# Optimization experiments

Measured on AMD Instinct MI355X. Metric: run time of the kernel, lower is better.

## Reference

```python
import jax, jax.numpy as jnp
import numpy as np

EPS_LN = 1e-5

def layer_norm(x, w, b):
    u = x.mean(-1, keepdims=True)
    s = jnp.mean((x - u) ** 2, -1, keepdims=True)
    return w * ((x - u) / jnp.sqrt(s + EPS_LN)) + b

def mlp(x, W, b, lw, lb):
    return jax.nn.relu(layer_norm(x @ W + b, lw, lb))

def mlp_gate(x, W, b, lw, lb):
    return jax.nn.sigmoid(layer_norm(x @ W + b, lw, lb))

def setup_inputs() -> dict:
    N, D = 768, 64
    key = jax.random.key(0)
    ks = jax.random.split(key, 12)
    inp = {
        'corr_index': jax.random.normal(ks[0], (N, N, 2), jnp.float32),
        'nei_index': jax.random.randint(ks[1], (N, N), 0, 2).astype(jnp.int64),
        'nei_num': jax.random.randint(ks[2], (N,), 0, N).astype(jnp.int64),
        'hidden_state': jax.random.normal(ks[3], (N, D), jnp.float32),
        'agent_v': jax.random.normal(ks[4], (N, 2), jnp.float32),
        # relativeLayer: MLP(3, D)
        'rel_w': jax.random.normal(ks[5], (3, D), jnp.float32) * (1.0 / np.sqrt(3)),
        'rel_b': jnp.zeros((D,), jnp.float32),
        'rel_lw': jnp.ones((D,), jnp.float32),
        'rel_lb': jnp.zeros((D,), jnp.float32),
        # ngate: MLP_gate(3D, D)
        'ng_w': jax.random.normal(ks[6], (3 * D, D), jnp.float32) * (1.0 / np.sqrt(3 * D)),
        'ng_b': jnp.zeros((D,), jnp.float32),
        'ng_lw': jnp.ones((D,), jnp.float32),
        'ng_lb': jnp.zeros((D,), jnp.float32),
        # WAr: MLP(3D, 1) -- LayerNorm(1) is identity in the source
        'war_w': jax.random.normal(ks[7], (3 * D, 1), jnp.float32) * (1.0 / np.sqrt(3 * D)),
        'war_b': jnp.zeros((1,), jnp.float32),
        # weight: MLP(D, D)
        'wt_w': jax.random.normal(ks[8], (D, D), jnp.float32) * (1.0 / np.sqrt(D)),
        'wt_b': jnp.zeros((D,), jnp.float32),
        'wt_lw': jnp.ones((D,), jnp.float32),
        'wt_lb': jnp.zeros((D,), jnp.float32),
    }
    return inp

def reference(corr_index, nei_index, nei_num, hidden_state, agent_v,
              rel_w, rel_b, rel_lw, rel_lb,
              ng_w, ng_b, ng_lw, ng_lb,
              war_w, war_b,
              wt_w, wt_b, wt_lw, wt_lb):
    N, D = hidden_state.shape
    # pair layout: row i*N+j  (i = receiver row of the NxN grid, j = column)
    agent_vt = jnp.tile(agent_v, (N, 1))                     # [N*N, 2], row i*N+j -> agent_v[j]
    corr_t = corr_index.reshape(N * N, 2)
    dot = agent_vt[:, 0] * corr_t[:, 0] + agent_vt[:, 1] * corr_t[:, 1]
    judge = jnp.sum(agent_vt ** 2, -1)
    angle = dot / (jnp.sqrt(judge * jnp.sum(corr_t ** 2, -1)) + 1e-10)
    angle = jnp.where(judge == 0, -1.0, angle)
    corr3 = jnp.concatenate([corr_t, angle[:, None]], -1)    # [N*N, 3]

    r_t = mlp(corr3, rel_w, rel_b, rel_lw, rel_lb)           # [N*N, D]
    nei_inputs = jnp.tile(hidden_state, (N, 1))              # row i*N+j -> h[j]
    hi_t = jnp.repeat(hidden_state, N, axis=0)               # row i*N+j -> h[i]
    tmp = jnp.concatenate([r_t, hi_t, nei_inputs], 1)        # [N*N, 3D]

    mask = (nei_index.reshape(N * N) > 0)
    nGate = mlp_gate(tmp, ng_w, ng_b, ng_lw, ng_lb)          # [N*N, D]
    tt = jax.nn.relu(tmp @ war_w + war_b).reshape(-1)        # LayerNorm(1) == identity

    Pos = jnp.where(mask, tt, 0.0).reshape(N, N)
    Pos = jnp.where(Pos == 0, -10000.0, Pos)
    Pos = jax.nn.softmax(Pos, axis=1)
    Pos_t = Pos.reshape(-1)

    H = jnp.where(mask[:, None], nei_inputs * nGate * Pos_t[:, None], 0.0)
    H_sum = mlp(H.reshape(N, N, D).sum(1), wt_w, wt_b, wt_lw, wt_lb)
    return hidden_state + H_sum
```

## Files before the change

kernel.cpp:

```cpp
#include <hip/hip_runtime.h>
#include <math.h>

#define NN 768
#define DD 64
#define WPB 4
#define HALVES 3
#define JW (NN / HALVES)
#define NSUB 4
#define RSTRIDE 34
#define B1STR 12
#define PREBLKS 18
#define PSTRIDE 68

typedef _Float16 half8 __attribute__((ext_vector_type(8)));
typedef float    f32x4 __attribute__((ext_vector_type(4)));
typedef __fp16   p2f   __attribute__((ext_vector_type(2)));

union FragU { uint4 u4; unsigned int u[4]; half8 h; };
union PkU   { unsigned int u; p2f p; };

__device__ __forceinline__ unsigned int pk2(float a, float b) {
    PkU t; t.p = __builtin_amdgcn_cvt_pkrtz(a, b); return t.u;
}
__device__ __forceinline__ float lane_bcast(float v, int src) {
    return __int_as_float(__builtin_amdgcn_readlane(__float_as_int(v), src));
}
__device__ __forceinline__ float rfl(float v) {
    return __int_as_float(__builtin_amdgcn_readfirstlane(__float_as_int(v)));
}
__device__ __forceinline__ f32x4 mfma16(FragU a, FragU b, f32x4 c) {
    return __builtin_amdgcn_mfma_f32_16x16x32_f16(a.h, b.h, c, 0, 0, 0);
}

__global__ __launch_bounds__(256) void k_prepack(
    const float* __restrict__ hs, const float* __restrict__ ng_w,
    const float* __restrict__ ng_b, const float* __restrict__ war_w,
    const float* __restrict__ war_b,
    const float* __restrict__ rel_w, const float* __restrict__ rel_b,
    const float* __restrict__ rel_lw, const float* __restrict__ rel_lb,
    float* __restrict__ sbase, float* __restrict__ warb, float* __restrict__ war3,
    unsigned int* __restrict__ hf16,
    unsigned int* __restrict__ afragS, unsigned int* __restrict__ afragR,
    float* __restrict__ mom)
{
    const int t = threadIdx.x, blk = blockIdx.x;
    const int lane = t & 63, q = t >> 6, g = lane >> 4, c16 = lane & 15;

    if (blk >= PREBLKS) {
        const int row = (blk - PREBLKS) * 4 + q;
        const float hv = hs[row * DD + lane];
        float a2 = ng_b[lane];
        #pragma unroll 8
        for (int k = 0; k < DD; ++k)
            a2 = fmaf(lane_bcast(hv, k), ng_w[(DD + k) * DD + lane], a2);
        sbase[row * DD + lane] = a2;
        float t2 = hv * war_w[DD + lane];
        float t3 = hv * war_w[2 * DD + lane];
        #pragma unroll
        for (int o = 32; o; o >>= 1) { t2 += __shfl_xor(t2, o); t3 += __shfl_xor(t3, o); }
        if (lane == 0) { warb[row] = t2 + war_b[0]; war3[row] = t3; }
        return;
    }

    for (int idx = blk * 256 + t; idx < NN * 32; idx += PREBLKS * 256) {
        const int row = idx >> 5, c = idx & 31;
        hf16[idx] = pk2(hs[row * DD + 2 * c], hs[row * DD + 2 * c + 1]);
    }

    if (blk < 16) {
        const int b = blk >> 2, c = blk & 3;
        const int dout = 16 * b + c16;
        const int k0 = 32 * c + g * 8 + 2 * q;
        const int r0 = (k0 < 64) ? k0 : (k0 + 64);
        afragS[(blk * 64 + lane) * 4 + q] =
            pk2(ng_w[r0 * DD + dout], ng_w[(r0 + 1) * DD + dout]);
    } else if (blk == 16) {
        const int b = q;
        const int d = 16 * b + c16;
        const float rlwd = rel_lw[d], rlbd = rel_lb[d];
        const float c0 = rel_w[d] * rlwd;
        const float c1 = rel_w[DD + d] * rlwd;
        const float c2 = rel_w[2 * DD + d] * rlwd;
        const float c3 = rel_b[d] * rlwd;
        PkU h01, h23, h45;
        h01.p = __builtin_amdgcn_cvt_pkrtz(c0, c1);
        h23.p = __builtin_amdgcn_cvt_pkrtz(c2, c3);
        h45.p = __builtin_amdgcn_cvt_pkrtz(rlwd, rlbd);
        const unsigned l01 = pk2(c0 - (float)h01.p[0], c1 - (float)h01.p[1]);
        const unsigned l23 = pk2(c2 - (float)h23.p[0], c3 - (float)h23.p[1]);
        const unsigned l45 = pk2(rlwd - (float)h45.p[0], rlbd - (float)h45.p[1]);
        const unsigned int base = (b * 64 + lane) * 4;
        unsigned v0, v1, v2;
        if (g == 0 || g == 1)      { v0 = h01.u; v1 = h23.u; v2 = h45.u; }
        else if (g == 2)           { v0 = l01;   v1 = l23;   v2 = l45;   }
        else                       { v0 = 0u;    v1 = 0u;    v2 = 0u;    }
        afragR[base + 0] = v0;
        afragR[base + 1] = v1;
        afragR[base + 2] = v2;
        afragR[base + 3] = 0u;
    } else {
        if (t < 64) {
            const float x0 = rel_w[t], x1 = rel_w[DD + t], x2 = rel_w[2 * DD + t];
            const float x3 = rel_b[t];
            float v[14] = {x0, x1, x2, x3,
                           x0 * x0, x1 * x1, x2 * x2, x3 * x3,
                           x0 * x1, x0 * x2, x0 * x3, x1 * x2, x1 * x3, x2 * x3};
            #pragma unroll
            for (int qq = 0; qq < 14; ++qq) {
                float s = v[qq];
                #pragma unroll
                for (int o = 32; o; o >>= 1) s += __shfl_xor(s, o);
                if (t == 0) mom[qq] = s * (1.f / 64.f);
            }
        }
    }
}

__global__ __launch_bounds__(64 * WPB) void k_main(
    const float* __restrict__ corr, const int* __restrict__ nei,
    const float* __restrict__ hs, const float* __restrict__ av,
    const float* __restrict__ ng_lw, const float* __restrict__ ng_lb,
    const float* __restrict__ war_w,
    const float* __restrict__ sbase, const float* __restrict__ warb,
    const float* __restrict__ war3,
    const unsigned int* __restrict__ afragS, const unsigned int* __restrict__ afragR,
    const unsigned int* __restrict__ hf16, const float* __restrict__ mom,
    float* __restrict__ part)
{
    const int h = blockIdx.x;
    const int i = blockIdx.y;
    const int tid = threadIdx.x;
    const int lane = tid & 63, wave = tid >> 6;
    const int g = lane >> 4, c16 = lane & 15;

    __shared__ uint4 sm_aS[16 * 64];
    __shared__ __align__(16) float sm_cst[4 * DD];
    __shared__ unsigned int sm_b1[WPB * 64 * B1STR];
    __shared__ unsigned int smr[WPB * 16 * RSTRIDE];
    __shared__ float sm_red[WPB][DD];
    __shared__ float sm_m[WPB], sm_l[WPB];

    for (int f = tid; f < 16 * 64; f += 64 * WPB)
        sm_aS[f] = ((const uint4*)afragS)[f];
    {
        const int a = tid >> 6, d = tid & 63;
        float v;
        if (a == 0)      v = sbase[i * DD + d];
        else if (a == 1) v = war_w[d];
        else if (a == 2) v = ng_lw[d];
        else             v = ng_lb[d];
        sm_cst[a * DD + d] = v;
    }

    FragU aR[4];
    #pragma unroll
    for (int b = 0; b < 4; ++b) aR[b].u4 = ((const uint4*)afragR)[b * 64 + lane];

    const float m0 = rfl(mom[0]), m1 = rfl(mom[1]), m2 = rfl(mom[2]), m3 = rfl(mom[3]);
    const float M00 = rfl(mom[4]), M11 = rfl(mom[5]), M22 = rfl(mom[6]), M33 = rfl(mom[7]);
    const float M01 = rfl(mom[8]), M02 = rfl(mom[9]), M03 = rfl(mom[10]);
    const float M12 = rfl(mom[11]), M13 = rfl(mom[12]), M23 = rfl(mom[13]);
    const float warbase = rfl(warb[i]);

    unsigned int* wrbase = smr + (wave * 16 + c16) * RSTRIDE;

    __syncthreads();

    const int jwbase = h * JW + wave * 64;
    {
        const int j = jwbase + lane;
        const float2 cc = ((const float2*)corr)[i * NN + j];
        const float2 vv = ((const float2*)av)[j];
        const float cx = cc.x, cy = cc.y;
        const float judge = vv.x * vv.x + vv.y * vv.y;
        const float dotv = fmaf(vv.x, cx, vv.y * cy);
        const float cn = cx * cx + cy * cy;
        float angle = __fdividef(dotv, sqrtf(judge * cn) + 1e-10f);
        if (judge == 0.f) angle = -1.f;

        const float u = fmaf(cx, m0, fmaf(cy, m1, fmaf(angle, m2, m3)));
        float e2 = M33;
        e2 = fmaf(cx * cx, M00, e2);
        e2 = fmaf(cy * cy, M11, e2);
        e2 = fmaf(angle * angle, M22, e2);
        e2 = fmaf(2.f * cx, fmaf(cy, M01, fmaf(angle, M02, M03)), e2);
        e2 = fmaf(2.f * cy, fmaf(angle, M12, M13), e2);
        e2 = fmaf(2.f * angle, M23, e2);
        const float vare = (e2 - u * u) + 1e-5f;
        const float inv = rsqrtf(vare);

        const float xc0 = cx * inv, xc1 = cy * inv, xc2 = angle * inv;
        const float xc3 = inv, xc4 = -u * inv;
        PkU s01, s23, s45;
        s01.p = __builtin_amdgcn_cvt_pkrtz(xc0, xc1);
        s23.p = __builtin_amdgcn_cvt_pkrtz(xc2, xc3);
        s45.p = __builtin_amdgcn_cvt_pkrtz(xc4, 1.f);
        const unsigned l0 = pk2(xc0 - (float)s01.p[0], xc1 - (float)s01.p[1]);
        const unsigned l1 = pk2(xc2 - (float)s23.p[0], xc3 - (float)s23.p[1]);
        const unsigned l2 = pk2(xc4 - (float)s45.p[0], 0.f);

        unsigned int* bp = sm_b1 + (wave * 64 + lane) * B1STR;
        *(uint4*)(bp)     = make_uint4(s01.u, s23.u, s45.u, 0u);
        *(uint4*)(bp + 4) = make_uint4(l0, l1, l2, 0u);
    }

    float acc[16];
    #pragma unroll
    for (int x = 0; x < 16; ++x) acc[x] = 0.f;
    float mrun = -INFINITY, lrun = 0.f;

    unsigned zofs = 0;

    #pragma unroll 1
    for (int s = 0; s < NSUB; ++s) {
        asm volatile("" : "+v"(zofs));
        const uint4* aSp = sm_aS + zofs;
        const float* cst = sm_cst + zofs;

        const int jj = jwbase + 16 * s + c16;
        const int    nv = nei[i * NN + jj];
        const float  w3 = war3[jj];
        FragU bx2, bx3;
        bx2.u4 = *(const uint4*)(hf16 + jj * 32 + 4 * g);
        bx3.u4 = *(const uint4*)(hf16 + jj * 32 + 16 + 4 * g);

        FragU b1;
        {
            const unsigned int* bp =
                sm_b1 + (wave * 64 + 16 * s + c16) * B1STR + ((g == 1) ? 4 : 0);
            const uint4 w = *(const uint4*)bp;
            b1.u[0] = (g == 3) ? 0u : w.x;
            b1.u[1] = (g == 3) ? 0u : w.y;
            b1.u[2] = (g == 3) ? 0u : w.z;
            b1.u[3] = 0u;
        }

        const f32x4 Z = {0.f, 0.f, 0.f, 0.f};
        float wd = 0.f;
        #pragma unroll
        for (int b = 0; b < 4; ++b) {
            const f32x4 P = mfma16(aR[b], b1, Z);
            const f32x4 wv = *(const f32x4*)(cst + 1 * DD + 16 * b + 4 * g);
            const float r0f = fmaxf(P[0], 0.f);
            const float r1f = fmaxf(P[1], 0.f);
            const float r2f = fmaxf(P[2], 0.f);
            const float r3f = fmaxf(P[3], 0.f);
            wd = fmaf(r0f, wv[0], wd);
            wd = fmaf(r1f, wv[1], wd);
            wd = fmaf(r2f, wv[2], wd);
            wd = fmaf(r3f, wv[3], wd);
            uint2 wvv;
            wvv.x = pk2(r0f, r1f);
            wvv.y = pk2(r2f, r3f);
            *(uint2*)(wrbase + 8 * b + 2 * g) = wvv;
        }

        FragU bx0, bx1;
        {
            const uint2 lo0 = *(const uint2*)(wrbase + 4 * g);
            const uint2 hi0 = *(const uint2*)(wrbase + 4 * g + 2);
            bx0.u[0] = lo0.x; bx0.u[1] = lo0.y; bx0.u[2] = hi0.x; bx0.u[3] = hi0.y;
            const uint2 lo1 = *(const uint2*)(wrbase + 16 + 4 * g);
            const uint2 hi1 = *(const uint2*)(wrbase + 16 + 4 * g + 2);
            bx1.u[0] = lo1.x; bx1.u[1] = lo1.y; bx1.u[2] = hi1.x; bx1.u[3] = hi1.y;
        }

        const f32x4 hv0 = *(const f32x4*)(hs + jj * DD +  0 + 4 * g);
        const f32x4 hv1 = *(const f32x4*)(hs + jj * DD + 16 + 4 * g);
        const f32x4 hv2 = *(const f32x4*)(hs + jj * DD + 32 + 4 * g);
        const f32x4 hv3 = *(const f32x4*)(hs + jj * DD + 48 + 4 * g);

        wd += __shfl_xor(wd, 16);
        wd += __shfl_xor(wd, 32);

        f32x4 S[4];
        #pragma unroll
        for (int b = 0; b < 4; ++b) {
            f32x4 cinit = *(const f32x4*)(cst + 0 * DD + 16 * b + 4 * g);
            FragU a2f, a3f, a0f, a1f;
            a2f.u4 = aSp[(b * 4 + 2) * 64 + lane];
            a3f.u4 = aSp[(b * 4 + 3) * 64 + lane];
            a0f.u4 = aSp[(b * 4 + 0) * 64 + lane];
            a1f.u4 = aSp[(b * 4 + 1) * 64 + lane];
            cinit = mfma16(a2f, bx2, cinit);
            cinit = mfma16(a3f, bx3, cinit);
            cinit = mfma16(a0f, bx0, cinit);
            cinit = mfma16(a1f, bx1, cinit);
            S[b] = cinit;
        }

        float s1 = 0.f, s2 = 0.f;
        #pragma unroll
        for (int x = 0; x < 16; ++x) {
            const float sv = S[x >> 2][x & 3];
            s1 += sv; s2 = fmaf(sv, sv, s2);
        }
        s1 += __shfl_xor(s1, 16); s1 += __shfl_xor(s1, 32);
        s2 += __shfl_xor(s2, 16); s2 += __shfl_xor(s2, 32);
        const float u2 = s1 * (1.f / 64.f);
        const float var2 = fmaf(s2, 1.f / 64.f, -u2 * u2);
        const float inv2 = rsqrtf(var2 + 1e-5f);

        float tt = wd + w3 + warbase;
        tt = fmaxf(tt, 0.f);
        const bool msk = nv > 0;
        const float p = (msk && tt > 0.f) ? tt : -10000.f;

        const float mn = fmaxf(mrun, p);
        const float alpha = __expf(mrun - mn);
        const float e = __expf(p - mn);
        const float eacc = msk ? e : 0.f;
        lrun = fmaf(lrun, alpha, e);
        mrun = mn;

        #pragma unroll
        for (int b = 0; b < 4; ++b) {
            const f32x4 hvb = (b == 0) ? hv0 : (b == 1) ? hv1 : (b == 2) ? hv2 : hv3;
            const f32x4 lw = *(const f32x4*)(cst + 2 * DD + 16 * b + 4 * g);
            const f32x4 lb = *(const f32x4*)(cst + 3 * DD + 16 * b + 4 * g);
            #pragma unroll
            for (int r = 0; r < 4; ++r) {
                const float ngv = fmaf((S[b][r] - u2) * inv2, lw[r], lb[r]);
                const float gate = __fdividef(1.f, 1.f + __expf(-ngv));
                acc[b * 4 + r] = fmaf(acc[b * 4 + r], alpha, eacc * gate * hvb[r]);
            }
        }
    }

    #pragma unroll
    for (int o = 1; o <= 8; o <<= 1) {
        const float mo  = __shfl_xor(mrun, o);
        const float lo_ = __shfl_xor(lrun, o);
        const float M   = fmaxf(mrun, mo);
        const float a1  = __expf(mrun - M);
        const float a2  = __expf(mo - M);
        lrun = lrun * a1 + lo_ * a2;
        #pragma unroll
        for (int x = 0; x < 16; ++x) {
            const float ao = __shfl_xor(acc[x], o);
            acc[x] = acc[x] * a1 + ao * a2;
        }
        mrun = M;
    }
    if (c16 == 0) {
        #pragma unroll
        for (int b = 0; b < 4; ++b)
            #pragma unroll
            for (int r = 0; r < 4; ++r)
                sm_red[wave][16 * b + g * 4 + r] = acc[b * 4 + r];
        if (lane == 0) { sm_m[wave] = mrun; sm_l[wave] = lrun; }
    }
    __syncthreads();

    if (tid < DD) {
        float M = sm_m[0];
        #pragma unroll
        for (int w = 1; w < WPB; ++w) M = fmaxf(M, sm_m[w]);
        float L = 0.f, A = 0.f;
        #pragma unroll
        for (int w = 0; w < WPB; ++w) {
            const float f = __expf(sm_m[w] - M);
            L = fmaf(sm_l[w], f, L);
            A = fmaf(sm_red[w][tid], f, A);
        }
        float* p = part + (i * HALVES + h) * PSTRIDE;
        p[tid] = A;
        if (tid == 0) { p[64] = M; p[65] = L; }
    }
}

__global__ __launch_bounds__(64) void k_final(
    const float* __restrict__ hs, const float* __restrict__ part,
    const float* __restrict__ wt_w, const float* __restrict__ wt_b,
    const float* __restrict__ wt_lw, const float* __restrict__ wt_lb,
    float* __restrict__ out)
{
    const int i = blockIdx.x;
    const int tid = threadIdx.x;

    float ms[HALVES], ls[HALVES];
    float M = -INFINITY;
    #pragma unroll
    for (int hh = 0; hh < HALVES; ++hh) {
        const float* p = part + (i * HALVES + hh) * PSTRIDE;
        ms[hh] = p[64]; ls[hh] = p[65];
        M = fmaxf(M, ms[hh]);
    }
    float L = 0.f, A = 0.f;
    #pragma unroll
    for (int hh = 0; hh < HALVES; ++hh) {
        const float f = __expf(ms[hh] - M);
        L = fmaf(ls[hh], f, L);
        A = fmaf(part[(i * HALVES + hh) * PSTRIDE + tid], f, A);
    }
    const float Hv = A / L;

    float v = wt_b[tid];
    #pragma unroll 8
    for (int k = 0; k < DD; ++k)
        v = fmaf(lane_bcast(Hv, k), wt_w[k * DD + tid], v);
    float t1 = v, t2 = v * v;
    #pragma unroll
    for (int o = 32; o; o >>= 1) { t1 += __shfl_xor(t1, o); t2 += __shfl_xor(t2, o); }
    const float uo = t1 * (1.f / 64.f);
    const float varo = fmaf(t2, 1.f / 64.f, -uo * uo);
    const float invo = rsqrtf(varo + 1e-5f);
    const float ro = fmaf((v - uo) * invo, wt_lw[tid], wt_lb[tid]);
    out[i * DD + tid] = hs[i * DD + tid] + fmaxf(ro, 0.f);
}

extern "C" void kernel_launch(void* const* d_in, const int* in_sizes, int n_in,
                              void* d_out, int out_size, void* d_ws, size_t ws_size,
                              hipStream_t stream) {
    const float* corr   = (const float*)d_in[0];
    const int*   nei    = (const int*)  d_in[1];
    const float* hs     = (const float*)d_in[3];
    const float* av     = (const float*)d_in[4];
    const float* rel_w  = (const float*)d_in[5];
    const float* rel_b  = (const float*)d_in[6];
    const float* rel_lw = (const float*)d_in[7];
    const float* rel_lb = (const float*)d_in[8];
    const float* ng_w   = (const float*)d_in[9];
    const float* ng_b   = (const float*)d_in[10];
    const float* ng_lw  = (const float*)d_in[11];
    const float* ng_lb  = (const float*)d_in[12];
    const float* war_w  = (const float*)d_in[13];
    const float* war_b  = (const float*)d_in[14];
    const float* wt_w   = (const float*)d_in[15];
    const float* wt_b   = (const float*)d_in[16];
    const float* wt_lw  = (const float*)d_in[17];
    const float* wt_lb  = (const float*)d_in[18];
    float* out = (float*)d_out;

    float* ws    = (float*)d_ws;
    float* sbase = ws;
    float* warb  = sbase + NN * DD;
    float* war3  = warb + NN;
    float* mom   = war3 + NN;
    unsigned int* hf16   = (unsigned int*)(mom + 16);
    unsigned int* afragS = hf16 + NN * 32;
    unsigned int* afragR = afragS + 16 * 64 * 4;
    float* part  = (float*)(afragR + 4 * 64 * 4);

    k_prepack<<<PREBLKS + NN / 4, 256, 0, stream>>>(
        hs, ng_w, ng_b, war_w, war_b, rel_w, rel_b, rel_lw, rel_lb,
        sbase, warb, war3, hf16, afragS, afragR, mom);
    k_main<<<dim3(HALVES, NN), 64 * WPB, 0, stream>>>(
        corr, nei, hs, av, ng_lw, ng_lb, war_w, sbase, warb, war3,
        afragS, afragR, hf16, mom, part);
    k_final<<<NN, 64, 0, stream>>>(
        hs, part, wt_w, wt_b, wt_lw, wt_lb, out);
}
```

Baseline: 144.9 us.

## Fuse final MLP into main kernel via last-block atomic counter

Removes the separate k_final launch. Each k_main block increments a per-row counter, and the last block for that row merges the softmax partials and runs the output MLP and LayerNorm. The counters are zeroed in the prepack kernel. It also splits the padded b1 shared buffer into two uint4 arrays and refactors the LayerNorm and gate arithmetic into fewer ops. The cost is a threadfence and atomic per block, plus a serial tail on the last block of each row.

```diff
diff --git a/kernel.cpp b/kernel.cpp
--- a/kernel.cpp
+++ b/kernel.cpp
@@ -8,7 +8,6 @@
 #define JW (NN / HALVES)
 #define NSUB 4
 #define RSTRIDE 34
-#define B1STR 12
 #define PREBLKS 18
 #define PSTRIDE 68
 
@@ -41,7 +40,7 @@
     float* __restrict__ sbase, float* __restrict__ warb, float* __restrict__ war3,
     unsigned int* __restrict__ hf16,
     unsigned int* __restrict__ afragS, unsigned int* __restrict__ afragR,
-    float* __restrict__ mom)
+    float* __restrict__ mom, unsigned int* __restrict__ cnt)
 {
     const int t = threadIdx.x, blk = blockIdx.x;
     const int lane = t & 63, q = t >> 6, g = lane >> 4, c16 = lane & 15;
@@ -99,6 +98,7 @@
         afragR[base + 2] = v2;
         afragR[base + 3] = 0u;
     } else {
+        for (int idx = t; idx < NN; idx += 256) cnt[idx] = 0u;
         if (t < 64) {
             const float x0 = rel_w[t], x1 = rel_w[DD + t], x2 = rel_w[2 * DD + t];
             const float x3 = rel_b[t];
@@ -125,7 +125,10 @@
     const float* __restrict__ war3,
     const unsigned int* __restrict__ afragS, const unsigned int* __restrict__ afragR,
     const unsigned int* __restrict__ hf16, const float* __restrict__ mom,
-    float* __restrict__ part)
+    float* __restrict__ part, unsigned int* __restrict__ cnt,
+    const float* __restrict__ wt_w, const float* __restrict__ wt_b,
+    const float* __restrict__ wt_lw, const float* __restrict__ wt_lb,
+    float* __restrict__ out)
 {
     const int h = blockIdx.x;
     const int i = blockIdx.y;
@@ -135,10 +138,12 @@
 
     __shared__ uint4 sm_aS[16 * 64];
     __shared__ __align__(16) float sm_cst[4 * DD];
-    __shared__ unsigned int sm_b1[WPB * 64 * B1STR];
+    __shared__ uint4 sm_b1h[WPB * 64];
+    __shared__ uint4 sm_b1l[WPB * 64];
     __shared__ unsigned int smr[WPB * 16 * RSTRIDE];
     __shared__ float sm_red[WPB][DD];
     __shared__ float sm_m[WPB], sm_l[WPB];
+    __shared__ unsigned int sm_last;
 
     for (int f = tid; f < 16 * 64; f += 64 * WPB)
         sm_aS[f] = ((const uint4*)afragS)[f];
@@ -199,9 +204,8 @@
         const unsigned l1 = pk2(xc2 - (float)s23.p[0], xc3 - (float)s23.p[1]);
         const unsigned l2 = pk2(xc4 - (float)s45.p[0], 0.f);
 
-        unsigned int* bp = sm_b1 + (wave * 64 + lane) * B1STR;
-        *(uint4*)(bp)     = make_uint4(s01.u, s23.u, s45.u, 0u);
-        *(uint4*)(bp + 4) = make_uint4(l0, l1, l2, 0u);
+        sm_b1h[wave * 64 + lane] = make_uint4(s01.u, s23.u, s45.u, 0u);
+        sm_b1l[wave * 64 + lane] = make_uint4(l0, l1, l2, 0u);
     }
 
     float acc[16];
@@ -226,9 +230,8 @@
 
         FragU b1;
         {
-            const unsigned int* bp =
-                sm_b1 + (wave * 64 + 16 * s + c16) * B1STR + ((g == 1) ? 4 : 0);
-            const uint4 w = *(const uint4*)bp;
+            const int bi = wave * 64 + 16 * s + c16;
+            const uint4 w = (g == 1) ? sm_b1l[bi] : sm_b1h[bi];
             b1.u[0] = (g == 3) ? 0u : w.x;
             b1.u[1] = (g == 3) ? 0u : w.y;
             b1.u[2] = (g == 3) ? 0u : w.z;
@@ -320,9 +323,12 @@
             const f32x4 lb = *(const f32x4*)(cst + 3 * DD + 16 * b + 4 * g);
             #pragma unroll
             for (int r = 0; r < 4; ++r) {
-                const float ngv = fmaf((S[b][r] - u2) * inv2, lw[r], lb[r]);
+                const float ilw = inv2 * lw[r];
+                const float blb = fmaf(-u2, ilw, lb[r]);
+                const float ngv = fmaf(S[b][r], ilw, blb);
                 const float gate = __fdividef(1.f, 1.f + __expf(-ngv));
-                acc[b * 4 + r] = fmaf(acc[b * 4 + r], alpha, eacc * gate * hvb[r]);
+                const float ehv = eacc * hvb[r];
+                acc[b * 4 + r] = fmaf(acc[b * 4 + r], alpha, gate * ehv);
             }
         }
     }
@@ -367,46 +373,46 @@
         p[tid] = A;
         if (tid == 0) { p[64] = M; p[65] = L; }
     }
-}
-
-__global__ __launch_bounds__(64) void k_final(
-    const float* __restrict__ hs, const float* __restrict__ part,
-    const float* __restrict__ wt_w, const float* __restrict__ wt_b,
-    const float* __restrict__ wt_lw, const float* __restrict__ wt_lb,
-    float* __restrict__ out)
-{
-    const int i = blockIdx.x;
-    const int tid = threadIdx.x;
-
-    float ms[HALVES], ls[HALVES];
-    float M = -INFINITY;
-    #pragma unroll
-    for (int hh = 0; hh < HALVES; ++hh) {
-        const float* p = part + (i * HALVES + hh) * PSTRIDE;
-        ms[hh] = p[64]; ls[hh] = p[65];
-        M = fmaxf(M, ms[hh]);
-    }
-    float L = 0.f, A = 0.f;
-    #pragma unroll
-    for (int hh = 0; hh < HALVES; ++hh) {
-        const float f = __expf(ms[hh] - M);
-        L = fmaf(ls[hh], f, L);
-        A = fmaf(part[(i * HALVES + hh) * PSTRIDE + tid], f, A);
-    }
-    const float Hv = A / L;
-
-    float v = wt_b[tid];
-    #pragma unroll 8
-    for (int k = 0; k < DD; ++k)
-        v = fmaf(lane_bcast(Hv, k), wt_w[k * DD + tid], v);
-    float t1 = v, t2 = v * v;
-    #pragma unroll
-    for (int o = 32; o; o >>= 1) { t1 += __shfl_xor(t1, o); t2 += __shfl_xor(t2, o); }
-    const float uo = t1 * (1.f / 64.f);
-    const float varo = fmaf(t2, 1.f / 64.f, -uo * uo);
-    const float invo = rsqrtf(varo + 1e-5f);
-    const float ro = fmaf((v - uo) * invo, wt_lw[tid], wt_lb[tid]);
-    out[i * DD + tid] = hs[i * DD + tid] + fmaxf(ro, 0.f);
+
+    __threadfence();
+    __syncthreads();
+    if (tid == 0)
+        sm_last = (atomicAdd(&cnt[i], 1u) == HALVES - 1) ? 1u : 0u;
+    __syncthreads();
+    if (sm_last) {
+        __threadfence();
+        if (tid < DD) {
+            float ms[HALVES], ls[HALVES];
+            float M = -INFINITY;
+            #pragma unroll
+            for (int hh = 0; hh < HALVES; ++hh) {
+                const float* p = part + (i * HALVES + hh) * PSTRIDE;
+                ms[hh] = p[64]; ls[hh] = p[65];
+                M = fmaxf(M, ms[hh]);
+            }
+            float L = 0.f, A = 0.f;
+            #pragma unroll
+            for (int hh = 0; hh < HALVES; ++hh) {
+                const float f = __expf(ms[hh] - M);
+                L = fmaf(ls[hh], f, L);
+                A = fmaf(part[(i * HALVES + hh) * PSTRIDE + tid], f, A);
+            }
+            const float Hv = A / L;
+
+            float v = wt_b[tid];
+            #pragma unroll 8
+            for (int k = 0; k < DD; ++k)
+                v = fmaf(lane_bcast(Hv, k), wt_w[k * DD + tid], v);
+            float t1 = v, t2 = v * v;
+            #pragma unroll
+            for (int o = 32; o; o >>= 1) { t1 += __shfl_xor(t1, o); t2 += __shfl_xor(t2, o); }
+            const float uo = t1 * (1.f / 64.f);
+            const float varo = fmaf(t2, 1.f / 64.f, -uo * uo);
+            const float invo = rsqrtf(varo + 1e-5f);
+            const float ro = fmaf((v - uo) * invo, wt_lw[tid], wt_lb[tid]);
+            out[i * DD + tid] = hs[i * DD + tid] + fmaxf(ro, 0.f);
+        }
+    }
 }
 
 extern "C" void kernel_launch(void* const* d_in, const int* in_sizes, int n_in,
@@ -441,13 +447,13 @@
     unsigned int* afragS = hf16 + NN * 32;
     unsigned int* afragR = afragS + 16 * 64 * 4;
     float* part  = (float*)(afragR + 4 * 64 * 4);
+    unsigned int* cnt = (unsigned int*)(part + NN * HALVES * PSTRIDE);
 
     k_prepack<<<PREBLKS + NN / 4, 256, 0, stream>>>(
         hs, ng_w, ng_b, war_w, war_b, rel_w, rel_b, rel_lw, rel_lb,
-        sbase, warb, war3, hf16, afragS, afragR, mom);
+        sbase, warb, war3, hf16, afragS, afragR, mom, cnt);
     k_main<<<dim3(HALVES, NN), 64 * WPB, 0, stream>>>(
         corr, nei, hs, av, ng_lw, ng_lb, war_w, sbase, warb, war3,
-        afragS, afragR, hf16, mom, part);
-    k_final<<<NN, 64, 0, stream>>>(
-        hs, part, wt_w, wt_b, wt_lw, wt_lb, out);
-}
+        afragS, afragR, hf16, mom, part, cnt,
+        wt_w, wt_b, wt_lw, wt_lb, out);
+}
```

Result: slower. 402.2 us (+177.5%).
